# Optimization experiments

Hardware: AMD Instinct MI355X
Metric: run time of the kernel (lower is better)

Reference implementation:

```python
import jax, jax.numpy as jnp
import numpy as np

B, N, H = 8, 1024, 768
NH, HD = 12, 64  # num heads, head size
E = 131072       # total edges (avg degree 16)
N_REL = 30


def setup_inputs() -> dict:
    key = jax.random.key(0)
    ks = jax.random.split(key, 8)
    node_states = jax.random.normal(ks[0], (B, N, H), dtype=jnp.float32)
    eb = jax.random.randint(ks[1], (E,), 0, B, dtype=jnp.int32)
    ei = jax.random.randint(ks[2], (E,), 0, N, dtype=jnp.int32)
    ej = jax.random.randint(ks[3], (E,), 0, N, dtype=jnp.int32)
    er = jax.random.randint(ks[4], (E,), 0, N_REL, dtype=jnp.int32)
    edge_indices = jnp.stack([eb, ei, ej, er], axis=0)  # (4, E)
    scale = 1.0 / np.sqrt(H)
    Wq = jax.random.normal(ks[5], (H, H), dtype=jnp.float32) * scale
    Wk = jax.random.normal(ks[6], (H, H), dtype=jnp.float32) * scale
    Wv = jax.random.normal(ks[7], (H, H), dtype=jnp.float32) * scale
    return {"node_states": node_states, "edge_indices": edge_indices,
            "Wq": Wq, "Wk": Wk, "Wv": Wv}


def reference(node_states, edge_indices, Wq, Wk, Wv):
    # node_states: (B, N, H); edge_indices: (4, E) rows = (batch, head_node, tail_node, relation)
    b, i, j = edge_indices[0], edge_indices[1], edge_indices[2]
    q = (node_states @ Wq).reshape(B, N, NH, HD)
    k = (node_states @ Wk).reshape(B, N, NH, HD)
    v = (node_states @ Wv).reshape(B, N, NH, HD)
    qe = q[b, i]  # (E, NH, HD) gather at head nodes
    ke = k[b, j]  # (E, NH, HD) gather at tail nodes
    scores = jnp.einsum('ehd,ehd->eh', qe, ke) * (1.0 / np.sqrt(HD))  # (E, NH)
    seg = b * N + i  # segment = (batch, head_node)
    nseg = B * N
    smax = jax.ops.segment_max(scores, seg, num_segments=nseg)  # (nseg, NH)
    ex = jnp.exp(scores - smax[seg])
    denom = jax.ops.segment_sum(ex, seg, num_segments=nseg)
    probs = ex / jnp.maximum(denom[seg], 1e-9)  # (E, NH) edge softmax over tail nodes
    ve = v[b, j]  # (E, NH, HD)
    out_e = (probs[:, :, None] * ve).reshape(E, NH * HD)
    out = jax.ops.segment_sum(out_e, seg, num_segments=nseg)  # sum over tail dim
    return out.reshape(B, N, H)
```

## Files before the change

### kernel.cpp

```cpp
#include <hip/hip_runtime.h>

#define BB 8
#define NN 1024
#define HH 768
#define NHEAD 12
#define HD 64
#define NSEG 8192
#define QKVN 2304
#define MAXDEG 64

typedef unsigned short u16;
typedef __attribute__((ext_vector_type(8))) short bf16x8;
typedef __attribute__((ext_vector_type(4))) float f32x4;

__device__ __forceinline__ float bf2f(u16 v) {
  return __uint_as_float(((unsigned)v) << 16);
}
__device__ __forceinline__ u16 f2bf(float f) {
  unsigned u = __float_as_uint(f);
  u += 0x7FFFu + ((u >> 16) & 1u);
  return (u16)(u >> 16);
}

__global__ void cast_x_kernel(const float* __restrict__ X, u16* __restrict__ Xb) {
  int i = blockIdx.x * blockDim.x + threadIdx.x;
  float4 f = ((const float4*)X)[i];
  ushort4 o;
  o.x = f2bf(f.x); o.y = f2bf(f.y); o.z = f2bf(f.z); o.w = f2bf(f.w);
  ((ushort4*)Xb)[i] = o;
}

__global__ void transpose_w_kernel(const float* __restrict__ Wq,
                                   const float* __restrict__ Wk,
                                   const float* __restrict__ Wv,
                                   u16* __restrict__ Wt) {
  __shared__ float tile[32][33];
  int n0 = blockIdx.x * 32;
  int k0 = blockIdx.y * 32;
  const float* W = (n0 < HH) ? Wq : (n0 < 2 * HH ? Wk : Wv);
  int nb = n0 - (n0 < HH ? 0 : (n0 < 2 * HH ? HH : 2 * HH));
  int tx = threadIdx.x, ty = threadIdx.y;
#pragma unroll
  for (int r = 0; r < 4; ++r)
    tile[ty + 8 * r][tx] = W[(k0 + ty + 8 * r) * HH + nb + tx];
  __syncthreads();
#pragma unroll
  for (int r = 0; r < 4; ++r)
    Wt[(n0 + ty + 8 * r) * HH + k0 + tx] = f2bf(tile[tx][ty + 8 * r]);
}

__global__ void build_kernel(const int* __restrict__ EI, int* __restrict__ cursor,
                             int* __restrict__ tailrow, int E) {
  int e = blockIdx.x * blockDim.x + threadIdx.x;
  if (e >= E) return;
  int b = EI[e];
  int seg = b * NN + EI[E + e];
  int j = EI[2 * E + e];
  int pos = atomicAdd(&cursor[seg], 1);
  if (pos < MAXDEG) tailrow[seg * MAXDEG + pos] = b * NN + j;
}

#define BM 128
#define BN 128
#define BK 32

__global__ __launch_bounds__(256) void gemm_kernel(const u16* __restrict__ Xb,
                                                   const u16* __restrict__ Wt,
                                                   u16* __restrict__ QKV) {
  __shared__ u16 As[2][BM * BK];
  __shared__ u16 Bs[2][BN * BK];
  const int tid = threadIdx.x;
  const int wave = tid >> 6;
  const int lane = tid & 63;
  const int m0 = blockIdx.y * BM;
  const int n0 = blockIdx.x * BN;
  const int wr = wave >> 1;
  const int wc = wave & 1;
  const int quad = lane >> 4;
  const int l15 = lane & 15;

  f32x4 acc[4][4] = {};

  const int srow = wave * 16 + (lane >> 2);
  const int scol = (lane & 3) * 8;

  auto stage = [&](int buf, int kt) {
#pragma unroll
    for (int p = 0; p < 2; ++p) {
      const u16* ga = Xb + (m0 + p * 64 + srow) * HH + kt + scol;
      const u16* gb = Wt + (n0 + p * 64 + srow) * HH + kt + scol;
      u16* la = As[buf] + p * 2048 + wave * 512;
      u16* lb = Bs[buf] + p * 2048 + wave * 512;
      __builtin_amdgcn_global_load_lds(
          (const __attribute__((address_space(1))) unsigned int*)(unsigned long long)ga,
          (__attribute__((address_space(3))) unsigned int*)(unsigned long long)la, 16, 0, 0);
      __builtin_amdgcn_global_load_lds(
          (const __attribute__((address_space(1))) unsigned int*)(unsigned long long)gb,
          (__attribute__((address_space(3))) unsigned int*)(unsigned long long)lb, 16, 0, 0);
    }
  };

  stage(0, 0);
  int buf = 0;
  for (int kt = 0; kt < HH; kt += BK) {
    __syncthreads();
    if (kt + BK < HH) stage(buf ^ 1, kt + BK);

    bf16x8 afr[4], bfr[4];
#pragma unroll
    for (int mi = 0; mi < 4; ++mi)
      afr[mi] = *(const bf16x8*)(As[buf] + (wr * 64 + mi * 16 + l15) * BK + quad * 8);
#pragma unroll
    for (int ni = 0; ni < 4; ++ni)
      bfr[ni] = *(const bf16x8*)(Bs[buf] + (wc * 64 + ni * 16 + l15) * BK + quad * 8);
#pragma unroll
    for (int mi = 0; mi < 4; ++mi)
#pragma unroll
      for (int ni = 0; ni < 4; ++ni)
        acc[mi][ni] = __builtin_amdgcn_mfma_f32_16x16x32_bf16(afr[mi], bfr[ni], acc[mi][ni], 0, 0, 0);
    buf ^= 1;
  }

#pragma unroll
  for (int mi = 0; mi < 4; ++mi)
#pragma unroll
    for (int ni = 0; ni < 4; ++ni) {
      int col = n0 + wc * 64 + ni * 16 + l15;
#pragma unroll
      for (int r = 0; r < 4; ++r) {
        int row = m0 + wr * 64 + mi * 16 + quad * 4 + r;
        QKV[row * QKVN + col] = f2bf(acc[mi][ni][r]);
      }
    }
}

__global__ __launch_bounds__(256) void attn_kernel(const u16* __restrict__ QKV,
                                                   const int* __restrict__ tailrow,
                                                   const int* __restrict__ cursor,
                                                   float* __restrict__ out) {
  __shared__ float sm[2 * 16 * 64];
  const int wv = threadIdx.x >> 6;
  const int lane = threadIdx.x & 63;
  const int sIb = wv >> 1;
  const int half = wv & 1;
  const int seg = blockIdx.x * 2 + sIb;
  const int base = seg * MAXDEG;
  int cnt = cursor[seg];
  if (cnt > MAXDEG) cnt = MAXDEG;
  const int myn = (cnt > half) ? ((cnt - half + 1) >> 1) : 0;

  const u16* qrow = QKV + seg * QKVN;
  float qv1[8], qv2[4];
  {
    bf16x8 q1 = *(const bf16x8*)(qrow + lane * 8);
    ushort4 q2 = *(const ushort4*)(qrow + 512 + lane * 4);
#pragma unroll
    for (int i = 0; i < 8; ++i) qv1[i] = bf2f((u16)q1[i]) * 0.125f;
    qv2[0] = bf2f(q2.x) * 0.125f; qv2[1] = bf2f(q2.y) * 0.125f;
    qv2[2] = bf2f(q2.z) * 0.125f; qv2[3] = bf2f(q2.w) * 0.125f;
  }

  float m1 = -__builtin_inff(), l1 = 0.f;
  float m2 = -__builtin_inff(), l2 = 0.f;
  float o1[8] = {}, o2[4] = {};

  auto loadkv = [&](int row, bf16x8& k1, ushort4& k2, bf16x8& v1, ushort4& v2) {
    const u16* kp = QKV + row * QKVN + HH;
    k1 = *(const bf16x8*)(kp + lane * 8);
    k2 = *(const ushort4*)(kp + 512 + lane * 4);
    v1 = *(const bf16x8*)(kp + HH + lane * 8);
    v2 = *(const ushort4*)(kp + HH + 512 + lane * 4);
  };

  if (myn > 0) {
    bf16x8 k1, v1, k1n, v1n;
    ushort4 k2, v2, k2n, v2n;
    loadkv(tailrow[base + half], k1, k2, v1, v2);
    for (int t = 0; t < myn; ++t) {
      int tn = (t + 1 < myn) ? t + 1 : t;
      loadkv(tailrow[base + half + 2 * tn], k1n, k2n, v1n, v2n);

      float s1 = 0.f;
#pragma unroll
      for (int i = 0; i < 8; ++i) s1 += qv1[i] * bf2f((u16)k1[i]);
      s1 += __shfl_xor(s1, 1, 64);
      s1 += __shfl_xor(s1, 2, 64);
      s1 += __shfl_xor(s1, 4, 64);
      float s2 = qv2[0] * bf2f(k2.x) + qv2[1] * bf2f(k2.y) +
                 qv2[2] * bf2f(k2.z) + qv2[3] * bf2f(k2.w);
      s2 += __shfl_xor(s2, 1, 64);
      s2 += __shfl_xor(s2, 2, 64);
      s2 += __shfl_xor(s2, 4, 64);
      s2 += __shfl_xor(s2, 8, 64);

      {
        float mn = fmaxf(m1, s1);
        float al = __expf(m1 - mn);
        float ex = __expf(s1 - mn);
        l1 = l1 * al + ex;
#pragma unroll
        for (int i = 0; i < 8; ++i) o1[i] = o1[i] * al + ex * bf2f((u16)v1[i]);
        m1 = mn;
      }
      {
        float mn = fmaxf(m2, s2);
        float al = __expf(m2 - mn);
        float ex = __expf(s2 - mn);
        l2 = l2 * al + ex;
        o2[0] = o2[0] * al + ex * bf2f(v2.x);
        o2[1] = o2[1] * al + ex * bf2f(v2.y);
        o2[2] = o2[2] * al + ex * bf2f(v2.z);
        o2[3] = o2[3] * al + ex * bf2f(v2.w);
        m2 = mn;
      }
      k1 = k1n; k2 = k2n; v1 = v1n; v2 = v2n;
    }
  }

  float* sb = sm + sIb * 16 * 64;
  if (half == 1) {
    sb[0 * 64 + lane] = m1;  sb[1 * 64 + lane] = l1;
    sb[2 * 64 + lane] = m2;  sb[3 * 64 + lane] = l2;
#pragma unroll
    for (int i = 0; i < 8; ++i) sb[(4 + i) * 64 + lane] = o1[i];
#pragma unroll
    for (int i = 0; i < 4; ++i) sb[(12 + i) * 64 + lane] = o2[i];
  }
  __syncthreads();
  if (half == 0) {
    float mB1 = sb[0 * 64 + lane], lB1 = sb[1 * 64 + lane];
    float mB2 = sb[2 * 64 + lane], lB2 = sb[3 * 64 + lane];

    float res1[8], res2[4];
    {
      float mn = fmaxf(fmaxf(m1, mB1), -1e30f);
      float aA = __expf(m1 - mn), aB = __expf(mB1 - mn);
      float l = l1 * aA + lB1 * aB;
      float inv = 1.f / fmaxf(l, 1e-9f);
#pragma unroll
      for (int i = 0; i < 8; ++i)
        res1[i] = (o1[i] * aA + sb[(4 + i) * 64 + lane] * aB) * inv;
    }
    {
      float mn = fmaxf(fmaxf(m2, mB2), -1e30f);
      float aA = __expf(m2 - mn), aB = __expf(mB2 - mn);
      float l = l2 * aA + lB2 * aB;
      float inv = 1.f / fmaxf(l, 1e-9f);
#pragma unroll
      for (int i = 0; i < 4; ++i)
        res2[i] = (o2[i] * aA + sb[(12 + i) * 64 + lane] * aB) * inv;
    }

    float* op = out + seg * HH;
    float4 r0 = {res1[0], res1[1], res1[2], res1[3]};
    float4 r1 = {res1[4], res1[5], res1[6], res1[7]};
    float4 r2 = {res2[0], res2[1], res2[2], res2[3]};
    ((float4*)(op + lane * 8))[0] = r0;
    ((float4*)(op + lane * 8))[1] = r1;
    *(float4*)(op + 512 + lane * 4) = r2;
  }
}

extern "C" void kernel_launch(void* const* d_in, const int* in_sizes, int n_in,
                              void* d_out, int out_size, void* d_ws, size_t ws_size,
                              hipStream_t stream) {
  const float* X  = (const float*)d_in[0];
  const int*   EI = (const int*)d_in[1];
  const float* Wq = (const float*)d_in[2];
  const float* Wk = (const float*)d_in[3];
  const float* Wv = (const float*)d_in[4];
  float* out = (float*)d_out;
  const int E = in_sizes[1] / 4;

  char* ws = (char*)d_ws;
  int* cursor  = (int*)(ws);
  int* tailrow = (int*)(ws + 32768);
  u16* Xb      = (u16*)(ws + 2129920);
  u16* Wt      = (u16*)(ws + 14712832);
  u16* QKV     = (u16*)(ws + 18251776);

  hipMemsetAsync(cursor, 0, NSEG * 4, stream);

  cast_x_kernel<<<(NSEG * HH / 4) / 256, 256, 0, stream>>>(X, Xb);
  transpose_w_kernel<<<dim3(QKVN / 32, HH / 32), dim3(32, 8), 0, stream>>>(Wq, Wk, Wv, Wt);
  build_kernel<<<(E + 255) / 256, 256, 0, stream>>>(EI, cursor, tailrow, E);
  gemm_kernel<<<dim3(QKVN / BN, NSEG / BM), 256, 0, stream>>>(Xb, Wt, QKV);
  attn_kernel<<<NSEG / 2, 256, 0, stream>>>(QKV, tailrow, cursor, out);
}
```

Before: 187.9 us.

## Triple-buffer GEMM with vmcnt waits, fold cursor memset, remap attention blocks

The GEMM main loop moves from a double-buffered LDS pipeline to a triple-buffered one. It replaces __syncthreads with explicit s_waitcnt vmcnt plus s_barrier, so two tiles stay in flight and more global-load latency is hidden. The separate hipMemsetAsync of the cursor array is folded into the cast kernel, removing one launch. The attention kernel now maps block indices to segments with an interleaved XCD-style swizzle, which changes cache locality across dies. The hand-written waitcnt depends on the exact count of outstanding loads and risks races if the compiler reorders or adds memory ops.

```diff
diff --git a/kernel.cpp b/kernel.cpp
--- a/kernel.cpp
+++ b/kernel.cpp
@@ -22,8 +22,10 @@
   return (u16)(u >> 16);
 }
 
-__global__ void cast_x_kernel(const float* __restrict__ X, u16* __restrict__ Xb) {
+__global__ void cast_x_kernel(const float* __restrict__ X, u16* __restrict__ Xb,
+                              int* __restrict__ cursor) {
   int i = blockIdx.x * blockDim.x + threadIdx.x;
+  if (blockIdx.x < NSEG / 256) cursor[blockIdx.x * 256 + threadIdx.x] = 0;
   float4 f = ((const float4*)X)[i];
   ushort4 o;
   o.x = f2bf(f.x); o.y = f2bf(f.y); o.z = f2bf(f.z); o.w = f2bf(f.w);
@@ -63,12 +65,13 @@
 #define BM 128
 #define BN 128
 #define BK 32
+#define NITER (HH / BK)
 
 __global__ __launch_bounds__(256) void gemm_kernel(const u16* __restrict__ Xb,
                                                    const u16* __restrict__ Wt,
                                                    u16* __restrict__ QKV) {
-  __shared__ u16 As[2][BM * BK];
-  __shared__ u16 Bs[2][BN * BK];
+  __shared__ u16 As[3][BM * BK];
+  __shared__ u16 Bs[3][BN * BK];
   const int tid = threadIdx.x;
   const int wave = tid >> 6;
   const int lane = tid & 63;
@@ -101,24 +104,31 @@
   };
 
   stage(0, 0);
-  int buf = 0;
-  for (int kt = 0; kt < HH; kt += BK) {
-    __syncthreads();
-    if (kt + BK < HH) stage(buf ^ 1, kt + BK);
-
+  stage(1, BK);
+
+#pragma unroll 3
+  for (int it = 0; it < NITER; ++it) {
+    if (it != NITER - 1) {
+      asm volatile("s_waitcnt vmcnt(4)" ::: "memory");
+    } else {
+      asm volatile("s_waitcnt vmcnt(0)" ::: "memory");
+    }
+    asm volatile("s_barrier" ::: "memory");
+    if (it + 2 < NITER) stage((it + 2) % 3, (it + 2) * BK);
+
+    const int b = it % 3;
     bf16x8 afr[4], bfr[4];
 #pragma unroll
     for (int mi = 0; mi < 4; ++mi)
-      afr[mi] = *(const bf16x8*)(As[buf] + (wr * 64 + mi * 16 + l15) * BK + quad * 8);
+      afr[mi] = *(const bf16x8*)(As[b] + (wr * 64 + mi * 16 + l15) * BK + quad * 8);
 #pragma unroll
     for (int ni = 0; ni < 4; ++ni)
-      bfr[ni] = *(const bf16x8*)(Bs[buf] + (wc * 64 + ni * 16 + l15) * BK + quad * 8);
+      bfr[ni] = *(const bf16x8*)(Bs[b] + (wc * 64 + ni * 16 + l15) * BK + quad * 8);
 #pragma unroll
     for (int mi = 0; mi < 4; ++mi)
 #pragma unroll
       for (int ni = 0; ni < 4; ++ni)
         acc[mi][ni] = __builtin_amdgcn_mfma_f32_16x16x32_bf16(afr[mi], bfr[ni], acc[mi][ni], 0, 0, 0);
-    buf ^= 1;
   }
 
 #pragma unroll
@@ -143,7 +153,8 @@
   const int lane = threadIdx.x & 63;
   const int sIb = wv >> 1;
   const int half = wv & 1;
-  const int seg = blockIdx.x * 2 + sIb;
+  const int blk = (blockIdx.x & 7) * (NSEG / 16) + (blockIdx.x >> 3);
+  const int seg = blk * 2 + sIb;
   const int base = seg * MAXDEG;
   int cnt = cursor[seg];
   if (cnt > MAXDEG) cnt = MAXDEG;
@@ -279,9 +290,7 @@
   u16* Wt      = (u16*)(ws + 14712832);
   u16* QKV     = (u16*)(ws + 18251776);
 
-  hipMemsetAsync(cursor, 0, NSEG * 4, stream);
-
-  cast_x_kernel<<<(NSEG * HH / 4) / 256, 256, 0, stream>>>(X, Xb);
+  cast_x_kernel<<<(NSEG * HH / 4) / 256, 256, 0, stream>>>(X, Xb, cursor);
   transpose_w_kernel<<<dim3(QKVN / 32, HH / 32), dim3(32, 8), 0, stream>>>(Wq, Wk, Wv, Wt);
   build_kernel<<<(E + 255) / 256, 256, 0, stream>>>(EI, cursor, tailrow, E);
   gemm_kernel<<<dim3(QKVN / BN, NSEG / BM), 256, 0, stream>>>(Xb, Wt, QKV);
```

Measured after the change: 177.1 us. -5.7%, faster.
